# Kernel tuning notes

Measured on AMD Instinct MI355X. Metric: run time of the kernel, lower is better.

## Reference

```python
import jax, jax.numpy as jnp
import numpy as np

N_NODES = 100000
N_EDGES = 1000000
D_FEAT = 128
N_ACTIONS = 64


def setup_inputs() -> dict:
    key = jax.random.key(0)
    ks = jax.random.split(key, 8)
    return {
        "x": jax.random.normal(ks[0], (N_NODES, D_FEAT), dtype=jnp.float32),
        "edge_index": jax.random.randint(ks[1], (2, N_EDGES), 0, N_NODES, dtype=jnp.int64),
        "W_gcn": jax.random.normal(ks[2], (D_FEAT, D_FEAT), dtype=jnp.float32) / np.sqrt(D_FEAT),
        "b_gcn": jax.random.normal(ks[3], (D_FEAT,), dtype=jnp.float32) * 0.02,
        "W_high": jax.random.normal(ks[4], (D_FEAT, N_ACTIONS), dtype=jnp.float32) / np.sqrt(D_FEAT),
        "b_high": jax.random.normal(ks[5], (N_ACTIONS,), dtype=jnp.float32) * 0.02,
        "W_low": jax.random.normal(ks[6], (D_FEAT, N_ACTIONS), dtype=jnp.float32) / np.sqrt(D_FEAT),
        "b_low": jax.random.normal(ks[7], (N_ACTIONS,), dtype=jnp.float32) * 0.02,
    }


def gcn_conv(x, edge_index, W, b):
    """PyG GCNConv: add self-loops, symmetric normalization, aggregate, linear."""
    n = x.shape[0]
    loops = jnp.arange(n, dtype=edge_index.dtype)
    src = jnp.concatenate([edge_index[0], loops])  # message sources
    dst = jnp.concatenate([edge_index[1], loops])  # message targets
    # degree of each target node (edge weight 1, incl. self-loop)
    deg = jax.ops.segment_sum(jnp.ones(src.shape[0], dtype=x.dtype), dst, num_segments=n)
    dinv = jax.lax.rsqrt(deg)  # deg >= 1 thanks to self-loops
    norm = dinv[src] * dinv[dst]  # [E+N]
    h = x @ W  # [N, D] dense transform first (cheaper than transforming messages)
    agg = jax.ops.segment_sum(h[src] * norm[:, None], dst, num_segments=n)
    return agg + b


def reference(x, edge_index, W_gcn, b_gcn, W_high, b_high, W_low, b_low):
    h = gcn_conv(x, edge_index, W_gcn, b_gcn)  # [N, D]
    high = h @ W_high + b_high  # [N, A]
    low = h @ W_low + b_low     # [N, A]
    return (high, low)
```

## Files before the change

### kernel.cpp

```cpp
#include <hip/hip_runtime.h>


#define BLOCK 256
#define BM 128
#define BK 32
#define SB 512
#define NB_MAX 784
#define CONV_BLOCKS 4096

__device__ inline unsigned short f2bf(float f) {
    unsigned u = __float_as_uint(f);
    unsigned r = (u + 0x7FFF + ((u >> 16) & 1)) >> 16;
    return (unsigned short)r;
}
__device__ inline float bf2f(unsigned short u) {
    return __uint_as_float(((unsigned)u) << 16);
}


__global__ __launch_bounds__(BLOCK) void k_prep(const float* __restrict__ x,
                                                const int* __restrict__ dst, int E,
                                                const float* __restrict__ Wg,
                                                const float* __restrict__ Wh,
                                                const float* __restrict__ Wl,
                                                const float* __restrict__ bg,
                                                const float* __restrict__ bh,
                                                const float* __restrict__ bl,
                                                float* __restrict__ Wf,
                                                float* __restrict__ bf,
                                                int* __restrict__ hist_g,
                                                unsigned short* __restrict__ xh,
                                                int n, int NB) {
    __shared__ int hist[NB_MAX];
    int b = blockIdx.x;
    if (b < 16) {
        int r = b * 8 + (threadIdx.x >> 5);
        int c0 = (threadIdx.x & 31) * 4;
        float a0 = 0.f, a1 = 0.f, a2 = 0.f, a3 = 0.f;
        for (int j = 0; j < 128; j++) {
            float wg = Wg[r * 128 + j];
            float4 wc;
            if (c0 < 64) wc = *(const float4*)(Wh + j * 64 + c0);
            else         wc = *(const float4*)(Wl + j * 64 + (c0 - 64));
            a0 += wg * wc.x; a1 += wg * wc.y; a2 += wg * wc.z; a3 += wg * wc.w;
        }
        *(float4*)(Wf + r * 128 + c0) = make_float4(a0, a1, a2, a3);
    } else if (b == 16) {
        int c = threadIdx.x;
        if (c < 128) {
            float acc = (c < 64) ? bh[c] : bl[c - 64];
            for (int j = 0; j < 128; j++) {
                float wc = (c < 64) ? Wh[j * 64 + c] : Wl[j * 64 + (c - 64)];
                acc += bg[j] * wc;
            }
            bf[c] = acc;
        }
    } else if (b < 17 + SB) {
        int blk = b - 17;
        for (int i = threadIdx.x; i < NB; i += BLOCK) hist[i] = 0;
        __syncthreads();
        int chunk = (E + SB - 1) / SB;
        int e0 = blk * chunk, e1 = min(E, e0 + chunk);
        for (int e = e0 + threadIdx.x; e < e1; e += BLOCK)
            atomicAdd(&hist[dst[e] >> 7], 1);
        __syncthreads();
        for (int i = threadIdx.x; i < NB; i += BLOCK)
            hist_g[(size_t)i * SB + blk] = hist[i];
    } else {
        const float4* x4 = (const float4*)x;
        ushort4* o4 = (ushort4*)xh;
        int total = n * 32;
        int i = (b - 17 - SB) * BLOCK + threadIdx.x;
        int stride = CONV_BLOCKS * BLOCK;
        for (; i < total; i += stride) {
            float4 v = x4[i];
            ushort4 o;
            o.x = f2bf(v.x); o.y = f2bf(v.y); o.z = f2bf(v.z); o.w = f2bf(v.w);
            o4[i] = o;
        }
    }
}


__global__ __launch_bounds__(BLOCK) void k_scanA(int* __restrict__ hist_g,
                                                 int* __restrict__ bucketTotal, int NB) {
    __shared__ int s[SB];
    int bkt = blockIdx.x;
    int t = threadIdx.x;
    int a0 = hist_g[(size_t)bkt * SB + t];
    int a1 = hist_g[(size_t)bkt * SB + t + 256];
    s[t] = a0; s[t + 256] = a1;
    __syncthreads();
    for (int ofs = 1; ofs < SB; ofs <<= 1) {
        int v0 = (t >= ofs) ? s[t - ofs] : 0;
        int v1 = (t + 256 >= ofs) ? s[t + 256 - ofs] : 0;
        __syncthreads();
        s[t] += v0; s[t + 256] += v1;
        __syncthreads();
    }
    hist_g[(size_t)bkt * SB + t] = s[t] - a0;
    hist_g[(size_t)bkt * SB + t + 256] = s[t + 256] - a1;
    if (t == 255) bucketTotal[bkt] = s[SB - 1];
}


__global__ __launch_bounds__(1024) void k_scanB(const int* __restrict__ bucketTotal,
                                                int* __restrict__ bucketStart,
                                                int NB, int E) {
    __shared__ int s[1024];
    int t = threadIdx.x;
    int v = (t < NB) ? bucketTotal[t] : 0;
    s[t] = v;
    __syncthreads();
    for (int ofs = 1; ofs < 1024; ofs <<= 1) {
        int u = (t >= ofs) ? s[t - ofs] : 0;
        __syncthreads();
        s[t] += u;
        __syncthreads();
    }
    if (t < NB) bucketStart[t] = s[t] - v;
    if (t == NB - 1) bucketStart[NB] = E;
}


__global__ __launch_bounds__(BLOCK) void k_scatter(const int* __restrict__ src,
                                                   const int* __restrict__ dst, int E,
                                                   const int* __restrict__ hist_g,
                                                   const int* __restrict__ bucketStart,
                                                   int2* __restrict__ ebuf, int NB) {
    __shared__ int cur[NB_MAX];
    int blk = blockIdx.x;
    for (int i = threadIdx.x; i < NB; i += BLOCK)
        cur[i] = bucketStart[i] + hist_g[(size_t)i * SB + blk];
    __syncthreads();
    int chunk = (E + SB - 1) / SB;
    int e0 = blk * chunk, e1 = min(E, e0 + chunk);
    for (int e = e0 + threadIdx.x; e < e1; e += BLOCK) {
        int d = dst[e];
        int pos = atomicAdd(&cur[d >> 7], 1);
        ebuf[pos] = make_int2(d, src[e]);
    }
}


__global__ __launch_bounds__(BLOCK) void k_node(const int2* __restrict__ ebuf,
                                                const int* __restrict__ bucketStart,
                                                int* __restrict__ off,
                                                float* __restrict__ dinv,
                                                int* __restrict__ csr,
                                                int n, int NB, int E) {
    __shared__ int cnt[128];
    __shared__ int pre[128];
    __shared__ int cur[128];
    int bkt = blockIdx.x;
    int t = threadIdx.x;
    int node0 = bkt << 7;
    int nn = min(128, n - node0);
    int eb0 = bucketStart[bkt], eb1 = bucketStart[bkt + 1];

    if (t < 128) cnt[t] = 0;
    __syncthreads();
    for (int e = eb0 + t; e < eb1; e += BLOCK)
        atomicAdd(&cnt[ebuf[e].x & 127], 1);
    __syncthreads();
    if (t < 128) pre[t] = cnt[t];
    __syncthreads();
    for (int ofs = 1; ofs < 128; ofs <<= 1) {
        int v = (t < 128 && t >= ofs) ? pre[t - ofs] : 0;
        __syncthreads();
        if (t < 128) pre[t] += v;
        __syncthreads();
    }
    if (t < 128) cur[t] = pre[t] - cnt[t];
    __syncthreads();
    if (t < nn) {
        off[node0 + t] = eb0 + cur[t];
        dinv[node0 + t] = rsqrtf((float)(cnt[t] + 1));
    }
    if (bkt == 0 && t == 0) off[n] = E;
    for (int e = eb0 + t; e < eb1; e += BLOCK) {
        int2 p = ebuf[e];
        int pos = atomicAdd(&cur[p.x & 127], 1);
        csr[eb0 + pos] = p.y;
    }
}


__global__ __launch_bounds__(BLOCK) void k_gather(const int* __restrict__ off,
                                                  const int* __restrict__ csr,
                                                  const float* __restrict__ dinv,
                                                  const unsigned short* __restrict__ xh,
                                                  const float* __restrict__ x,
                                                  float* __restrict__ aggx, int n) {
    int wave = (blockIdx.x * blockDim.x + threadIdx.x) >> 6;
    int lane = threadIdx.x & 63;
    if (wave >= n) return;
    int d = wave;
    int beg = off[d], end = off[d + 1];

    float accx = 0.f, accy = 0.f;
    for (int base = beg; base < end; base += 64) {
        int cnt = min(64, end - base);
        int s = 0; float w = 0.f;
        if (lane < cnt) { s = csr[base + lane]; w = dinv[s]; }
        int j = 0;
        for (; j + 4 <= cnt; j += 4) {
            int s0 = __shfl(s, j);
            int s1 = __shfl(s, j + 1);
            int s2 = __shfl(s, j + 2);
            int s3 = __shfl(s, j + 3);
            float w0 = __shfl(w, j);
            float w1 = __shfl(w, j + 1);
            float w2 = __shfl(w, j + 2);
            float w3 = __shfl(w, j + 3);
            ushort2 v0 = ((const ushort2*)(xh + (size_t)s0 * 128))[lane];
            ushort2 v1 = ((const ushort2*)(xh + (size_t)s1 * 128))[lane];
            ushort2 v2 = ((const ushort2*)(xh + (size_t)s2 * 128))[lane];
            ushort2 v3 = ((const ushort2*)(xh + (size_t)s3 * 128))[lane];
            accx += w0 * bf2f(v0.x) + w1 * bf2f(v1.x) + w2 * bf2f(v2.x) + w3 * bf2f(v3.x);
            accy += w0 * bf2f(v0.y) + w1 * bf2f(v1.y) + w2 * bf2f(v2.y) + w3 * bf2f(v3.y);
        }
        for (; j < cnt; j++) {
            int sj = __shfl(s, j);
            float wj = __shfl(w, j);
            ushort2 v = ((const ushort2*)(xh + (size_t)sj * 128))[lane];
            accx += wj * bf2f(v.x);
            accy += wj * bf2f(v.y);
        }
    }
    float dv = dinv[d];
    float2 xv = ((const float2*)(x + (size_t)d * 128))[lane];
    float2 o;
    o.x = dv * accx + dv * dv * xv.x;
    o.y = dv * accy + dv * dv * xv.y;
    ((float2*)(aggx + (size_t)d * 128))[lane] = o;
}


__global__ __launch_bounds__(BLOCK) void k_final(const float* __restrict__ aggx,
                                                 const float* __restrict__ Wf,
                                                 const float* __restrict__ bf,
                                                 float* __restrict__ out, int n) {
    __shared__ float Xs[BK][BM];
    __shared__ float Ws[BK][BM];
    int rg = threadIdx.x >> 3;
    int cg = threadIdx.x & 7;
    int row0 = blockIdx.x * BM;

    float acc[4][16];
#pragma unroll
    for (int r = 0; r < 4; r++)
#pragma unroll
        for (int j = 0; j < 16; j++) acc[r][j] = 0.f;

    for (int kt = 0; kt < 128; kt += BK) {
        int kt4 = kt >> 2;
#pragma unroll
        for (int i = 0; i < 4; i++) {
            int s = threadIdx.x + i * 256;
            int r = s >> 3;
            int c4 = s & 7;
            int gr = row0 + r;
            if (gr >= n) gr = n - 1;
            float4 v = ((const float4*)(aggx + (size_t)gr * 128))[kt4 + c4];
            Xs[c4 * 4 + 0][r] = v.x;
            Xs[c4 * 4 + 1][r] = v.y;
            Xs[c4 * 4 + 2][r] = v.z;
            Xs[c4 * 4 + 3][r] = v.w;
        }
#pragma unroll
        for (int i = 0; i < 4; i++) {
            int s = threadIdx.x + i * 256;
            int k = s >> 5;
            int c4 = s & 31;
            float4 v = ((const float4*)(Wf + (size_t)(kt + k) * 128))[c4];
            *(float4*)&Ws[k][c4 * 4] = v;
        }
        __syncthreads();

#pragma unroll 4
        for (int k = 0; k < BK; k++) {
            float xf[4];
            *(float4*)xf = *(const float4*)&Xs[k][rg * 4];
            float wf[16];
            const float4* wrow = (const float4*)&Ws[k][cg * 16];
            ((float4*)wf)[0] = wrow[0];
            ((float4*)wf)[1] = wrow[1];
            ((float4*)wf)[2] = wrow[2];
            ((float4*)wf)[3] = wrow[3];
#pragma unroll
            for (int r = 0; r < 4; r++)
#pragma unroll
                for (int j = 0; j < 16; j++) acc[r][j] += xf[r] * wf[j];
        }
        __syncthreads();
    }

    float bvf[16];
#pragma unroll
    for (int j4 = 0; j4 < 4; j4++)
        ((float4*)bvf)[j4] = ((const float4*)(bf + cg * 16))[j4];

#pragma unroll
    for (int r = 0; r < 4; r++) {
        int row = row0 + rg * 4 + r;
        if (row >= n) break;
        float* base = (cg < 4) ? (out + (size_t)row * 64 + cg * 16)
                               : (out + (size_t)n * 64 + (size_t)row * 64 + (cg - 4) * 16);
#pragma unroll
        for (int j4 = 0; j4 < 4; j4++) {
            float4 v = make_float4(acc[r][j4 * 4 + 0] + bvf[j4 * 4 + 0],
                                   acc[r][j4 * 4 + 1] + bvf[j4 * 4 + 1],
                                   acc[r][j4 * 4 + 2] + bvf[j4 * 4 + 2],
                                   acc[r][j4 * 4 + 3] + bvf[j4 * 4 + 3]);
            ((float4*)base)[j4] = v;
        }
    }
}

extern "C" void kernel_launch(void* const* d_in, const int* in_sizes, int n_in,
                              void* d_out, int out_size, void* d_ws, size_t ws_size,
                              hipStream_t stream) {
    const float* x  = (const float*)d_in[0];
    const int*   ei = (const int*)d_in[1];
    const float* Wg = (const float*)d_in[2];
    const float* bg = (const float*)d_in[3];
    const float* Wh = (const float*)d_in[4];
    const float* bh = (const float*)d_in[5];
    const float* Wl = (const float*)d_in[6];
    const float* bl = (const float*)d_in[7];
    float* out = (float*)d_out;

    int n = in_sizes[0] / 128;
    int E = in_sizes[1] / 2;
    const int* src = ei;
    const int* dst = ei + E;
    int NB = (n + 127) >> 7;

    char* ws = (char*)d_ws;
    int*   hist_g      = (int*)ws;                ws += (size_t)NB_MAX * SB * 4;
    int*   bucketTotal = (int*)ws;                ws += (size_t)NB_MAX * 4;
    int*   bucketStart = (int*)ws;                ws += (size_t)(NB_MAX + 1) * 4;
    int2*  ebuf        = (int2*)ws;               ws += (size_t)E * 8;
    int*   off         = (int*)ws;                ws += (size_t)(n + 1) * 4;
    float* dinv        = (float*)ws;              ws += (size_t)n * 4;
    int*   csr         = (int*)ws;                ws += (size_t)E * 4;
    float* aggx        = (float*)ws;              ws += (size_t)n * 128 * 4;
    float* Wf          = (float*)ws;              ws += (size_t)128 * 128 * 4;
    float* bf          = (float*)ws;              ws += (size_t)128 * 4;
    unsigned short* xh = (unsigned short*)ws;

    k_prep<<<17 + SB + CONV_BLOCKS, BLOCK, 0, stream>>>(
        x, dst, E, Wg, Wh, Wl, bg, bh, bl, Wf, bf, hist_g, xh, n, NB);
    k_scanA<<<NB, BLOCK, 0, stream>>>(hist_g, bucketTotal, NB);
    k_scanB<<<1, 1024, 0, stream>>>(bucketTotal, bucketStart, NB, E);
    k_scatter<<<SB, BLOCK, 0, stream>>>(src, dst, E, hist_g, bucketStart, ebuf, NB);
    k_node<<<NB, BLOCK, 0, stream>>>(ebuf, bucketStart, off, dinv, csr, n, NB, E);
    k_gather<<<((size_t)n * 64 + BLOCK - 1) / BLOCK, BLOCK, 0, stream>>>(
        off, csr, dinv, xh, x, aggx, n);
    k_final<<<(n + BM - 1) / BM, BLOCK, 0, stream>>>(aggx, Wf, bf, out, n);
}
```

Measured before the change: 300.9 us.

## Use fp16 MFMA for final projection with half-precision aggregated features

```diff
diff --git a/kernel.cpp b/kernel.cpp
--- a/kernel.cpp
+++ b/kernel.cpp
@@ -2,11 +2,13 @@
 
 
 #define BLOCK 256
-#define BM 128
-#define BK 32
 #define SB 512
 #define NB_MAX 784
 #define CONV_BLOCKS 4096
+
+typedef _Float16 half8 __attribute__((ext_vector_type(8)));
+typedef _Float16 half2v __attribute__((ext_vector_type(2)));
+typedef float f32x4 __attribute__((ext_vector_type(4)));
 
 __device__ inline unsigned short f2bf(float f) {
     unsigned u = __float_as_uint(f);
@@ -26,7 +28,7 @@
                                                 const float* __restrict__ bg,
                                                 const float* __restrict__ bh,
                                                 const float* __restrict__ bl,
-                                                float* __restrict__ Wf,
+                                                _Float16* __restrict__ WfT,
                                                 float* __restrict__ bf,
                                                 int* __restrict__ hist_g,
                                                 unsigned short* __restrict__ xh,
@@ -44,7 +46,10 @@
             else         wc = *(const float4*)(Wl + j * 64 + (c0 - 64));
             a0 += wg * wc.x; a1 += wg * wc.y; a2 += wg * wc.z; a3 += wg * wc.w;
         }
-        *(float4*)(Wf + r * 128 + c0) = make_float4(a0, a1, a2, a3);
+        WfT[(size_t)(c0 + 0) * 128 + r] = (_Float16)a0;
+        WfT[(size_t)(c0 + 1) * 128 + r] = (_Float16)a1;
+        WfT[(size_t)(c0 + 2) * 128 + r] = (_Float16)a2;
+        WfT[(size_t)(c0 + 3) * 128 + r] = (_Float16)a3;
     } else if (b == 16) {
         int c = threadIdx.x;
         if (c < 128) {
@@ -191,7 +196,7 @@
                                                   const float* __restrict__ dinv,
                                                   const unsigned short* __restrict__ xh,
                                                   const float* __restrict__ x,
-                                                  float* __restrict__ aggx, int n) {
+                                                  _Float16* __restrict__ aggh, int n) {
     int wave = (blockIdx.x * blockDim.x + threadIdx.x) >> 6;
     int lane = threadIdx.x & 63;
     if (wave >= n) return;
@@ -230,90 +235,67 @@
     }
     float dv = dinv[d];
     float2 xv = ((const float2*)(x + (size_t)d * 128))[lane];
-    float2 o;
-    o.x = dv * accx + dv * dv * xv.x;
-    o.y = dv * accy + dv * dv * xv.y;
-    ((float2*)(aggx + (size_t)d * 128))[lane] = o;
-}
-
-
-__global__ __launch_bounds__(BLOCK) void k_final(const float* __restrict__ aggx,
-                                                 const float* __restrict__ Wf,
+    half2v o;
+    o.x = (_Float16)(dv * accx + dv * dv * xv.x);
+    o.y = (_Float16)(dv * accy + dv * dv * xv.y);
+    ((half2v*)(aggh + (size_t)d * 128))[lane] = o;
+}
+
+
+__global__ __launch_bounds__(BLOCK) void k_final(const _Float16* __restrict__ aggh,
+                                                 const _Float16* __restrict__ WfT,
                                                  const float* __restrict__ bf,
                                                  float* __restrict__ out, int n) {
-    __shared__ float Xs[BK][BM];
-    __shared__ float Ws[BK][BM];
-    int rg = threadIdx.x >> 3;
-    int cg = threadIdx.x & 7;
-    int row0 = blockIdx.x * BM;
-
-    float acc[4][16];
-#pragma unroll
-    for (int r = 0; r < 4; r++)
-#pragma unroll
-        for (int j = 0; j < 16; j++) acc[r][j] = 0.f;
-
-    for (int kt = 0; kt < 128; kt += BK) {
-        int kt4 = kt >> 2;
-#pragma unroll
-        for (int i = 0; i < 4; i++) {
-            int s = threadIdx.x + i * 256;
-            int r = s >> 3;
-            int c4 = s & 7;
-            int gr = row0 + r;
-            if (gr >= n) gr = n - 1;
-            float4 v = ((const float4*)(aggx + (size_t)gr * 128))[kt4 + c4];
-            Xs[c4 * 4 + 0][r] = v.x;
-            Xs[c4 * 4 + 1][r] = v.y;
-            Xs[c4 * 4 + 2][r] = v.z;
-            Xs[c4 * 4 + 3][r] = v.w;
-        }
-#pragma unroll
-        for (int i = 0; i < 4; i++) {
-            int s = threadIdx.x + i * 256;
-            int k = s >> 5;
-            int c4 = s & 31;
-            float4 v = ((const float4*)(Wf + (size_t)(kt + k) * 128))[c4];
-            *(float4*)&Ws[k][c4 * 4] = v;
-        }
-        __syncthreads();
-
-#pragma unroll 4
-        for (int k = 0; k < BK; k++) {
-            float xf[4];
-            *(float4*)xf = *(const float4*)&Xs[k][rg * 4];
-            float wf[16];
-            const float4* wrow = (const float4*)&Ws[k][cg * 16];
-            ((float4*)wf)[0] = wrow[0];
-            ((float4*)wf)[1] = wrow[1];
-            ((float4*)wf)[2] = wrow[2];
-            ((float4*)wf)[3] = wrow[3];
-#pragma unroll
-            for (int r = 0; r < 4; r++)
-#pragma unroll
-                for (int j = 0; j < 16; j++) acc[r][j] += xf[r] * wf[j];
-        }
-        __syncthreads();
-    }
-
-    float bvf[16];
-#pragma unroll
-    for (int j4 = 0; j4 < 4; j4++)
-        ((float4*)bvf)[j4] = ((const float4*)(bf + cg * 16))[j4];
-
-#pragma unroll
-    for (int r = 0; r < 4; r++) {
-        int row = row0 + rg * 4 + r;
-        if (row >= n) break;
-        float* base = (cg < 4) ? (out + (size_t)row * 64 + cg * 16)
-                               : (out + (size_t)n * 64 + (size_t)row * 64 + (cg - 4) * 16);
-#pragma unroll
-        for (int j4 = 0; j4 < 4; j4++) {
-            float4 v = make_float4(acc[r][j4 * 4 + 0] + bvf[j4 * 4 + 0],
-                                   acc[r][j4 * 4 + 1] + bvf[j4 * 4 + 1],
-                                   acc[r][j4 * 4 + 2] + bvf[j4 * 4 + 2],
-                                   acc[r][j4 * 4 + 3] + bvf[j4 * 4 + 3]);
-            ((float4*)base)[j4] = v;
+    int wave = threadIdx.x >> 6;
+    int lane = threadIdx.x & 63;
+    int l15 = lane & 15;
+    int lk = lane >> 4;
+    int row_base = blockIdx.x * 128 + wave * 32;
+
+    half8 a[2][4];
+#pragma unroll
+    for (int rf = 0; rf < 2; rf++) {
+        int r = row_base + rf * 16 + l15;
+        if (r >= n) r = n - 1;
+        const _Float16* ap = aggh + (size_t)r * 128 + lk * 8;
+#pragma unroll
+        for (int kk = 0; kk < 4; kk++)
+            a[rf][kk] = *(const half8*)(ap + kk * 32);
+    }
+
+    f32x4 acc[2][8];
+#pragma unroll
+    for (int rf = 0; rf < 2; rf++)
+#pragma unroll
+        for (int cf = 0; cf < 8; cf++)
+            acc[rf][cf] = (f32x4){0.f, 0.f, 0.f, 0.f};
+
+#pragma unroll
+    for (int kk = 0; kk < 4; kk++) {
+#pragma unroll
+        for (int cf = 0; cf < 8; cf++) {
+            const _Float16* bp = WfT + (size_t)(cf * 16 + l15) * 128 + kk * 32 + lk * 8;
+            half8 bfr = *(const half8*)bp;
+#pragma unroll
+            for (int rf = 0; rf < 2; rf++)
+                acc[rf][cf] = __builtin_amdgcn_mfma_f32_16x16x32_f16(
+                    a[rf][kk], bfr, acc[rf][cf], 0, 0, 0);
+        }
+    }
+
+#pragma unroll
+    for (int cf = 0; cf < 8; cf++) {
+        int c = cf * 16 + l15;
+        float bv = bf[c];
+        size_t cbase = (c < 64) ? (size_t)c : (size_t)n * 64 + (size_t)(c - 64);
+#pragma unroll
+        for (int rf = 0; rf < 2; rf++) {
+            int r0 = row_base + rf * 16 + lk * 4;
+#pragma unroll
+            for (int j = 0; j < 4; j++) {
+                int r = r0 + j;
+                if (r < n) out[cbase + (size_t)r * 64] = acc[rf][cf][j] + bv;
+            }
         }
     }
 }
@@ -340,23 +322,23 @@
     char* ws = (char*)d_ws;
     int*   hist_g      = (int*)ws;                ws += (size_t)NB_MAX * SB * 4;
     int*   bucketTotal = (int*)ws;                ws += (size_t)NB_MAX * 4;
-    int*   bucketStart = (int*)ws;                ws += (size_t)(NB_MAX + 1) * 4;
+    int*   bucketStart = (int*)ws;                ws += (size_t)(NB_MAX + 2) * 4;
     int2*  ebuf        = (int2*)ws;               ws += (size_t)E * 8;
     int*   off         = (int*)ws;                ws += (size_t)(n + 1) * 4;
     float* dinv        = (float*)ws;              ws += (size_t)n * 4;
     int*   csr         = (int*)ws;                ws += (size_t)E * 4;
-    float* aggx        = (float*)ws;              ws += (size_t)n * 128 * 4;
-    float* Wf          = (float*)ws;              ws += (size_t)128 * 128 * 4;
+    _Float16* aggh     = (_Float16*)ws;           ws += (size_t)n * 128 * 2;
+    _Float16* WfT      = (_Float16*)ws;           ws += (size_t)128 * 128 * 2;
     float* bf          = (float*)ws;              ws += (size_t)128 * 4;
     unsigned short* xh = (unsigned short*)ws;
 
     k_prep<<<17 + SB + CONV_BLOCKS, BLOCK, 0, stream>>>(
-        x, dst, E, Wg, Wh, Wl, bg, bh, bl, Wf, bf, hist_g, xh, n, NB);
+        x, dst, E, Wg, Wh, Wl, bg, bh, bl, WfT, bf, hist_g, xh, n, NB);
     k_scanA<<<NB, BLOCK, 0, stream>>>(hist_g, bucketTotal, NB);
     k_scanB<<<1, 1024, 0, stream>>>(bucketTotal, bucketStart, NB, E);
     k_scatter<<<SB, BLOCK, 0, stream>>>(src, dst, E, hist_g, bucketStart, ebuf, NB);
     k_node<<<NB, BLOCK, 0, stream>>>(ebuf, bucketStart, off, dinv, csr, n, NB, E);
     k_gather<<<((size_t)n * 64 + BLOCK - 1) / BLOCK, BLOCK, 0, stream>>>(
-        off, csr, dinv, xh, x, aggx, n);
-    k_final<<<(n + BM - 1) / BM, BLOCK, 0, stream>>>(aggx, Wf, bf, out, n);
-}
+        off, csr, dinv, xh, x, aggh, n);
+    k_final<<<(n + 127) / 128, BLOCK, 0, stream>>>(aggh, WfT, bf, out, n);
+}
```

Measured after the change: 273.2 us. 9.2% less time.
